# Kernel tuning notes

Measured on AMD Instinct MI355X. Metric: run time of the kernel, lower is better.

## Reference

```python
import jax, jax.numpy as jnp
import numpy as np

EPS = 1e-5
NEG_SLOPE = 0.2
NUM_ITER = 3
C = 32            # channel
LCAPS = 40        # latent_caps_size
LVEC = 40         # latent_vec_size
PCAPS = 1287      # prim_caps_size (937 + 234 + 116)


def conv1d(x, w, stride, pad):
    # x: [B, Cin, L], w: [Cout, Cin, K]
    return jax.lax.conv_general_dilated(
        x, w, window_strides=(stride,), padding=[(pad, pad)],
        dimension_numbers=('NCH', 'OIH', 'NCH'))


def bn_lrelu(x, g, b, m, v):
    # eval-mode BatchNorm1d + LeakyReLU(0.2); x: [B, C, L]
    scale = (g * jax.lax.rsqrt(v + EPS))[None, :, None]
    y = (x - m[None, :, None]) * scale + b[None, :, None]
    return jnp.where(y >= 0, y, NEG_SLOPE * y)


def squash(t):
    sn = jnp.sum(t * t, axis=-1, keepdims=True)
    return sn * t / ((1.0 + sn) * jnp.sqrt(sn))


def setup_inputs() -> dict:
    key = jax.random.key(0)
    ks = jax.random.split(key, 10)
    data = jax.random.normal(ks[0], (32, 1, 4681), jnp.float32)
    conv1_w = 0.1 * jax.random.normal(ks[1], (C, 1, 5), jnp.float32)
    conv2_w = 0.1 * jax.random.normal(ks[2], (C, C, 5), jnp.float32)
    conv3_w = 0.1 * jax.random.normal(ks[3], (C, C, 4), jnp.float32)
    lin_w = 0.1 * jax.random.normal(ks[4], (C, C, 1), jnp.float32)
    bn_gamma = 1.0 + 0.1 * jax.random.normal(ks[5], (4, C), jnp.float32)
    bn_beta = 0.1 * jax.random.normal(ks[6], (4, C), jnp.float32)
    bn_mean = 0.1 * jax.random.normal(ks[7], (4, C), jnp.float32)
    bn_var = 0.5 + jax.random.uniform(ks[8], (4, C), jnp.float32)
    W_caps = 0.01 * jax.random.normal(ks[9], (LCAPS, PCAPS, LVEC, C), jnp.float32)
    return dict(data=data, conv1_w=conv1_w, conv2_w=conv2_w, conv3_w=conv3_w,
                lin_w=lin_w, bn_gamma=bn_gamma, bn_beta=bn_beta,
                bn_mean=bn_mean, bn_var=bn_var, W_caps=W_caps)


def reference(data, conv1_w, conv2_w, conv3_w, lin_w,
              bn_gamma, bn_beta, bn_mean, bn_var, W_caps):
    # OctreeKeyConv (eval mode: BN uses running stats, dropout off)
    x1 = bn_lrelu(conv1d(data, conv1_w, 5, 2), bn_gamma[0], bn_beta[0], bn_mean[0], bn_var[0])  # [B,32,937]
    x2 = bn_lrelu(conv1d(x1, conv2_w, 4, 0), bn_gamma[1], bn_beta[1], bn_mean[1], bn_var[1])    # [B,32,234]
    x3 = bn_lrelu(conv1d(x2, conv3_w, 2, 0), bn_gamma[2], bn_beta[2], bn_mean[2], bn_var[2])    # [B,32,116]
    x = jnp.concatenate([x1, x2, x3], axis=2)                                                    # [B,32,1287]
    x = bn_lrelu(conv1d(x, lin_w, 1, 0), bn_gamma[3], bn_beta[3], bn_mean[3], bn_var[3])
    x = jnp.transpose(x, (0, 2, 1))  # [B, 1287, 32]

    # LatentCapsLayer: u_hat[b,l,p,v] = sum_s W[l,p,v,s] x[b,p,s]
    u_hat = jnp.einsum('lpvs,bps->blpv', W_caps, x)  # [B,40,1287,40]
    u_det = jax.lax.stop_gradient(u_hat)
    B = x.shape[0]
    b_ij = jnp.zeros((B, LCAPS, PCAPS), x.dtype)
    v = None
    for it in range(NUM_ITER):
        c = jax.nn.softmax(b_ij, axis=1)  # softmax over latent caps
        if it == NUM_ITER - 1:
            v = squash(jnp.sum(c[..., None] * u_hat, axis=2, keepdims=True))  # [B,40,1,40]
        else:
            v = squash(jnp.sum(c[..., None] * u_det, axis=2, keepdims=True))
            b_ij = b_ij + jnp.sum(v * u_det, axis=-1)
    latent = jnp.squeeze(v, axis=2)       # [B,40,40]
    return jnp.sum(latent, axis=-1)       # [B,40]
```

## Files before the change

kernel.cpp:

```cpp
#include <hip/hip_runtime.h>

#define EPSB 1e-5f
#define NEG 0.2f

__device__ __forceinline__ float lrelu(float y) { return y >= 0.f ? y : NEG * y; }

typedef const __attribute__((address_space(1))) unsigned int gas1_u32;
typedef __attribute__((address_space(3))) unsigned int as3_u32;
__device__ __forceinline__ void gload16nt(const float* g, float* l) {
  __builtin_amdgcn_global_load_lds((gas1_u32*)g, (as3_u32*)l, 16, 0, 2);
}
#define WAITVM(N) asm volatile("s_waitcnt vmcnt(" #N ")" ::: "memory")

typedef float floatx4 __attribute__((ext_vector_type(4)));
typedef short bf16x8 __attribute__((ext_vector_type(8)));
__device__ __forceinline__ void nt_store4(float4 v, float* addr) {
  floatx4 w = {v.x, v.y, v.z, v.w};
  __builtin_nontemporal_store(w, (floatx4*)addr);
}

__device__ __forceinline__ unsigned short bfr(float f) {
  unsigned int b = __float_as_uint(f);
  return (unsigned short)((b + 0x7FFFu + ((b >> 16) & 1u)) >> 16);
}
__device__ __forceinline__ ushort4 f4bf(floatx4 a) {
  ushort4 r;
  r.x = bfr(a.x); r.y = bfr(a.y); r.z = bfr(a.z); r.w = bfr(a.w);
  return r;
}
__device__ __forceinline__ float4 bf4f(ushort4 h) {
  return make_float4(__uint_as_float((unsigned int)h.x << 16),
                     __uint_as_float((unsigned int)h.y << 16),
                     __uint_as_float((unsigned int)h.z << 16),
                     __uint_as_float((unsigned int)h.w << 16));
}

__device__ __forceinline__ void barrier_nodrain() {
  asm volatile("s_waitcnt lgkmcnt(0)" ::: "memory");
  __builtin_amdgcn_s_barrier();
  __builtin_amdgcn_sched_barrier(0);
}

__global__ __launch_bounds__(256) void k_front(
    const float* __restrict__ data, const float* __restrict__ w1,
    const float* __restrict__ w2, const float* __restrict__ w3,
    const float* __restrict__ lw, const float* __restrict__ bg,
    const float* __restrict__ bb, const float* __restrict__ bm,
    const float* __restrict__ bv, float* __restrict__ xt)
{
  __shared__ float x1s[32][132];
  __shared__ float x2s[32][40];
  __shared__ float x3s[32][20];
  const int b = blockIdx.x >> 3, q = blockIdx.x & 7, t = threadIdx.x;
  const int o1s = (937*q)/8, o1e = (937*(q+1))/8;
  const int o2s = (234*q)/8, o2e = (234*(q+1))/8;
  const int o3s = (116*q)/8, o3e = (116*(q+1))/8;
  int n2s = min(o2s, 2*o3s);
  int n2e = max(o2e, 2*(o3e-1)+4); if (n2e > 234) n2e = 234;
  int n1s = min(o1s, 4*n2s);
  int n1e = max(o1e, 4*(n2e-1)+5); if (n1e > 937) n1e = 937;
  const int w1w = n1e - n1s, w2w = n2e - n2s, w3w = o3e - o3s;

  for (int idx = t; idx < 32*w1w; idx += 256) {
    int c = idx / w1w, j = n1s + idx % w1w;
    float acc = 0.f;
    int base = 5*j - 2;
    #pragma unroll
    for (int k = 0; k < 5; ++k) {
      int pos = base + k;
      float d = (pos >= 0 && pos < 4681) ? data[b*4681 + pos] : 0.f;
      acc += w1[c*5 + k] * d;
    }
    float sc = bg[c] * rsqrtf(bv[c] + EPSB);
    x1s[c][j - n1s] = lrelu((acc - bm[c]) * sc + bb[c]);
  }
  __syncthreads();
  for (int idx = t; idx < 32*w2w; idx += 256) {
    int c = idx / w2w, j = n2s + idx % w2w;
    float acc = 0.f;
    int col = 4*j - n1s;
    for (int ci = 0; ci < 32; ++ci) {
      #pragma unroll
      for (int k = 0; k < 5; ++k) acc += w2[(c*32 + ci)*5 + k] * x1s[ci][col + k];
    }
    float sc = bg[32+c] * rsqrtf(bv[32+c] + EPSB);
    x2s[c][j - n2s] = lrelu((acc - bm[32+c]) * sc + bb[32+c]);
  }
  __syncthreads();
  for (int idx = t; idx < 32*w3w; idx += 256) {
    int c = idx / w3w, j = o3s + idx % w3w;
    float acc = 0.f;
    int col = 2*j - n2s;
    for (int ci = 0; ci < 32; ++ci) {
      #pragma unroll
      for (int k = 0; k < 4; ++k) acc += w3[(c*32 + ci)*4 + k] * x2s[ci][col + k];
    }
    float sc = bg[64+c] * rsqrtf(bv[64+c] + EPSB);
    x3s[c][j - o3s] = lrelu((acc - bm[64+c]) * sc + bb[64+c]);
  }
  __syncthreads();
  const int np1 = o1e - o1s, np2 = o2e - o2s, np3 = o3e - o3s;
  const int np = np1 + np2 + np3;
  for (int idx = t; idx < np*32; idx += 256) {
    int pi = idx >> 5, s = idx & 31;
    float acc = 0.f;
    int p;
    if (pi < np1) {
      int j = o1s + pi; p = j;
      int col = j - n1s;
      for (int ci = 0; ci < 32; ++ci) acc += lw[s*32 + ci] * x1s[ci][col];
    } else if (pi < np1 + np2) {
      int j = o2s + (pi - np1); p = 937 + j;
      int col = j - n2s;
      for (int ci = 0; ci < 32; ++ci) acc += lw[s*32 + ci] * x2s[ci][col];
    } else {
      int j = o3s + (pi - np1 - np2); p = 1171 + j;
      int col = j - o3s;
      for (int ci = 0; ci < 32; ++ci) acc += lw[s*32 + ci] * x3s[ci][col];
    }
    float sc = bg[96+s] * rsqrtf(bv[96+s] + EPSB);
    xt[p*1024 + b*32 + s] = lrelu((acc - bm[96+s]) * sc + bb[96+s]);
  }
}

__global__ __launch_bounds__(256) void k_uhat(
    const float* __restrict__ W, const float* __restrict__ xt,
    unsigned short* __restrict__ ubf, float* __restrict__ s0part)
{
  extern __shared__ float lds[];
  float* wbuf = lds;
  unsigned short* xs_hi = (unsigned short*)(lds + 10240);
  unsigned short* xs_lo = xs_hi + 10240;
  const int t = threadIdx.x;
  const int wv = t >> 6, lane = t & 63;
  const int wi = blockIdx.x*4 + wv;
  const int l = wi % 40, chunk = wi / 40;
  const int p0 = chunk * 8;
  float* myw = wbuf + wv * 2560;
  const float* Wl = W + (size_t)l * 1287 * 1280;
  const int row = lane & 15, g = lane >> 4;

  for (int idx = t; idx < 2048; idx += 256) {
    int pl = idx >> 8, rem = idx & 255;
    int b = rem >> 3, s4 = rem & 7;
    int pg = p0 + pl;
    float4 v = make_float4(0.f, 0.f, 0.f, 0.f);
    if (pg < 1287) v = *(const float4*)(xt + pg*1024 + b*32 + s4*4);
    unsigned int b0 = __float_as_uint(v.x), b1 = __float_as_uint(v.y);
    unsigned int b2 = __float_as_uint(v.z), b3 = __float_as_uint(v.w);
    ushort4 h, lo;
    h.x = (unsigned short)(b0 >> 16); h.y = (unsigned short)(b1 >> 16);
    h.z = (unsigned short)(b2 >> 16); h.w = (unsigned short)(b3 >> 16);
    lo.x = (unsigned short)(__float_as_uint(v.x - __uint_as_float(b0 & 0xffff0000u)) >> 16);
    lo.y = (unsigned short)(__float_as_uint(v.y - __uint_as_float(b1 & 0xffff0000u)) >> 16);
    lo.z = (unsigned short)(__float_as_uint(v.z - __uint_as_float(b2 & 0xffff0000u)) >> 16);
    lo.w = (unsigned short)(__float_as_uint(v.w - __uint_as_float(b3 & 0xffff0000u)) >> 16);
    int off = pl*1280 + b*40 + s4*4;
    *(ushort4*)(xs_hi + off) = h;
    *(ushort4*)(xs_lo + off) = lo;
  }
  #pragma unroll
  for (int i = 0; i < 5; ++i) {
    int gg = i*64 + lane, v = gg >> 3, s4 = (gg & 7) ^ (v & 7);
    gload16nt(Wl + (size_t)p0*1280 + (v*8 + s4)*4, myw + i*256);
  }
  #pragma unroll
  for (int i = 0; i < 5; ++i) {
    int gg = i*64 + lane, v = gg >> 3, s4 = (gg & 7) ^ (v & 7);
    gload16nt(Wl + (size_t)(p0+1)*1280 + (v*8 + s4)*4, myw + 1280 + i*256);
  }
  __syncthreads();

  floatx4 s0acc[2][3];
  #pragma unroll
  for (int mt = 0; mt < 2; ++mt)
    #pragma unroll
    for (int nt = 0; nt < 3; ++nt)
      s0acc[mt][nt] = (floatx4){0.f, 0.f, 0.f, 0.f};

  #pragma unroll
  for (int pp = 0; pp < 8; ++pp) {
    const int p = p0 + pp;
    if (p >= 1287) break;
    if (pp == 1)      WAITVM(11);
    else if (pp >= 2 && pp <= 6) WAITVM(17);
    else if (pp == 7) WAITVM(12);
    const float* wb = myw + (pp & 1)*1280;
    const unsigned short* xh = xs_hi + pp*1280;
    const unsigned short* xl = xs_lo + pp*1280;
    bf16x8 aH[2], aL[2];
    aH[0] = *(const bf16x8*)(xh + row*40 + g*8);
    aH[1] = *(const bf16x8*)(xh + (16 + row)*40 + g*8);
    aL[0] = *(const bf16x8*)(xl + row*40 + g*8);
    aL[1] = *(const bf16x8*)(xl + (16 + row)*40 + g*8);
    floatx4 acc[2][3];
    #pragma unroll
    for (int mt = 0; mt < 2; ++mt)
      #pragma unroll
      for (int nt = 0; nt < 3; ++nt)
        acc[mt][nt] = (floatx4){0.f, 0.f, 0.f, 0.f};
    #pragma unroll
    for (int nt = 0; nt < 3; ++nt) {
      int vq = nt*16 + row;
      bool valid = vq < 40;
      int vv = valid ? vq : 0;
      float4 w0 = *(const float4*)(wb + vv*32 + (((2*g) ^ (vv & 7)) << 2));
      float4 w1 = *(const float4*)(wb + vv*32 + (((2*g + 1) ^ (vv & 7)) << 2));
      float ws[8] = {w0.x, w0.y, w0.z, w0.w, w1.x, w1.y, w1.z, w1.w};
      bf16x8 bH, bL;
      #pragma unroll
      for (int j = 0; j < 8; ++j) {
        unsigned int bits = __float_as_uint(ws[j]);
        unsigned short hs = (unsigned short)(bits >> 16);
        float lf = ws[j] - __uint_as_float(bits & 0xffff0000u);
        unsigned short lsv = (unsigned short)(__float_as_uint(lf) >> 16);
        bH[j] = valid ? (short)hs : (short)0;
        bL[j] = valid ? (short)lsv : (short)0;
      }
      #pragma unroll
      for (int mt = 0; mt < 2; ++mt) {
        acc[mt][nt] = __builtin_amdgcn_mfma_f32_16x16x32_bf16(aH[mt], bH, acc[mt][nt], 0, 0, 0);
        acc[mt][nt] = __builtin_amdgcn_mfma_f32_16x16x32_bf16(aH[mt], bL, acc[mt][nt], 0, 0, 0);
        acc[mt][nt] = __builtin_amdgcn_mfma_f32_16x16x32_bf16(aL[mt], bH, acc[mt][nt], 0, 0, 0);
      }
    }
    if (pp < 6) {
      int psrc = p + 2; if (psrc > 1286) psrc = 1286;
      asm volatile("s_waitcnt lgkmcnt(0)" ::: "memory");
      __builtin_amdgcn_sched_barrier(0);
      #pragma unroll
      for (int i = 0; i < 5; ++i) {
        int gg = i*64 + lane, v = gg >> 3, s4 = (gg & 7) ^ (v & 7);
        gload16nt(Wl + (size_t)psrc*1280 + (v*8 + s4)*4, myw + (pp & 1)*1280 + i*256);
      }
    }
    #pragma unroll
    for (int mt = 0; mt < 2; ++mt)
      #pragma unroll
      for (int nt = 0; nt < 3; ++nt) {
        int vq = nt*16 + row;
        if (vq < 40) {
          int q4 = mt*4 + g;
          *(ushort4*)(ubf + ((size_t)(q4*1287 + p))*6400 + l*160 + vq*4) = f4bf(acc[mt][nt]);
          s0acc[mt][nt] += acc[mt][nt];
        }
      }
  }
  #pragma unroll
  for (int mt = 0; mt < 2; ++mt)
    #pragma unroll
    for (int nt = 0; nt < 3; ++nt) {
      int vq = nt*16 + row;
      if (vq < 40) {
        int q4 = mt*4 + g;
        *(floatx4*)(s0part + (size_t)chunk*51200 + l*1280 + vq*32 + q4*4) = s0acc[mt][nt];
      }
    }
}

__global__ __launch_bounds__(64) void k_squash0(
    const float* __restrict__ s0, float* __restrict__ v0t)
{
  const int b = blockIdx.x / 40, l = blockIdx.x % 40, t = threadIdx.x;
  float s = 0.f;
  if (t < 40) s = s0[(l*40 + t)*32 + b] * (1.f/40.f);
  float sq = s*s;
  #pragma unroll
  for (int d = 1; d < 64; d <<= 1) sq += __shfl_xor(sq, d);
  float scale = sq > 0.f ? sq / ((1.f + sq) * sqrtf(sq)) : 0.f;
  if (t < 40) v0t[((size_t)(b >> 2)*1600 + l*40 + t)*4 + (b & 3)] = s * scale;
}

__global__ __launch_bounds__(64) void k_squash1(
    const float* __restrict__ sred, const float* __restrict__ v0t,
    float* __restrict__ v1t, float* __restrict__ vsum)
{
  const int b = blockIdx.x / 40, l = blockIdx.x % 40, t = threadIdx.x;
  float s = 0.f;
  size_t off = ((size_t)(b >> 2)*1600 + l*40 + t)*4 + (b & 3);
  if (t < 40) s = sred[off];
  float sq = s*s;
  #pragma unroll
  for (int d = 1; d < 64; d <<= 1) sq += __shfl_xor(sq, d);
  float scale = sq > 0.f ? sq / ((1.f + sq) * sqrtf(sq)) : 0.f;
  if (t < 40) {
    float v1 = s * scale;
    v1t[off] = v1;
    vsum[off] = v0t[off] + v1;
  }
}

__global__ __launch_bounds__(64) void k_final(
    const float* __restrict__ sred, float* __restrict__ out)
{
  const int b = blockIdx.x / 40, l = blockIdx.x % 40, t = threadIdx.x;
  float s = 0.f;
  if (t < 40) s = sred[((size_t)(b >> 2)*1600 + l*40 + t)*4 + (b & 3)];
  float sq = s*s, ss = s;
  #pragma unroll
  for (int d = 1; d < 64; d <<= 1) { sq += __shfl_xor(sq, d); ss += __shfl_xor(ss, d); }
  float scale = sq > 0.f ? sq / ((1.f + sq) * sqrtf(sq)) : 0.f;
  if (t == 0) out[b*40 + l] = ss * scale;
}

#define RPC 13
#define NCHUNK 99
__global__ __launch_bounds__(400) void k_route7(
    const unsigned short* __restrict__ ubf, const float* __restrict__ vprev,
    float* __restrict__ spart, int rev)
{
  __shared__ float4 dred[400];
  __shared__ float dot_lds[160];
  __shared__ float c_lds[160];
  const int q4 = blockIdx.x & 7;
  const int chunk0 = blockIdx.x >> 3;
  const int chunk = rev ? (NCHUNK - 1 - chunk0) : chunk0;
  const int t = threadIdx.x;
  const int l = t / 10;
  const int p0 = chunk * RPC;
  const ushort4* u4 = (const ushort4*)ubf;
  const float4* vp4 = (const float4*)vprev + (size_t)q4*1600;

  float4 vv[4], s4[4];
  ushort4 uu[3][4];
  #pragma unroll
  for (int j = 0; j < 4; ++j) {
    vv[j] = vp4[t*4 + j];
    s4[j] = make_float4(0.f, 0.f, 0.f, 0.f);
  }
  {
    const ushort4* up0 = u4 + ((size_t)q4*1287 + p0)*1600;
    const ushort4* up1 = u4 + ((size_t)q4*1287 + p0 + 1)*1600;
    #pragma unroll
    for (int j = 0; j < 4; ++j) { uu[0][j] = up0[t*4 + j]; uu[1][j] = up1[t*4 + j]; }
  }

  #pragma unroll
  for (int pl = 0; pl < RPC; ++pl) {
    const int cur = pl % 3, pf = (pl + 2) % 3;
    const size_t qp = (size_t)q4*1287 + p0 + pl;
    float4 fu[4];
    #pragma unroll
    for (int j = 0; j < 4; ++j) fu[j] = bf4f(uu[cur][j]);
    float4 dp = make_float4(0.f, 0.f, 0.f, 0.f);
    #pragma unroll
    for (int j = 0; j < 4; ++j) {
      dp.x += fu[j].x*vv[j].x; dp.y += fu[j].y*vv[j].y;
      dp.z += fu[j].z*vv[j].z; dp.w += fu[j].w*vv[j].w;
    }
    dred[t] = dp;
    if (pl + 2 < RPC) {
      const ushort4* upn = u4 + (qp + 2)*1600;
      #pragma unroll
      for (int j = 0; j < 4; ++j) uu[pf][j] = upn[t*4 + j];
    }
    barrier_nodrain();
    if (t < 160) {
      const int lr = t >> 2, b4 = t & 3;
      float d = 0.f;
      #pragma unroll
      for (int vq = 0; vq < 10; ++vq)
        d += ((const float*)&dred[lr*10 + vq])[b4];
      dot_lds[b4*40 + lr] = d;
    }
    barrier_nodrain();
    if (t < 256) {
      const int b4 = t >> 6, ll = t & 63;
      float d = (ll < 40) ? dot_lds[b4*40 + ll] : -1e30f;
      float m = d;
      #pragma unroll
      for (int off = 32; off; off >>= 1) m = fmaxf(m, __shfl_xor(m, off));
      float e = expf(d - m);
      float Z = e;
      #pragma unroll
      for (int off = 32; off; off >>= 1) Z += __shfl_xor(Z, off);
      if (ll < 40) c_lds[b4*40 + ll] = e * (1.f / Z);
    }
    barrier_nodrain();
    {
      float c0 = c_lds[l], c1 = c_lds[40 + l], c2 = c_lds[80 + l], c3 = c_lds[120 + l];
      #pragma unroll
      for (int j = 0; j < 4; ++j) {
        s4[j].x += fu[j].x*c0; s4[j].y += fu[j].y*c1;
        s4[j].z += fu[j].z*c2; s4[j].w += fu[j].w*c3;
      }
    }
  }
  float* sp = spart + ((size_t)chunk*8 + q4)*6400;
  #pragma unroll
  for (int j = 0; j < 4; ++j)
    nt_store4(s4[j], sp + (t*4 + j)*4);
}

__global__ __launch_bounds__(256) void k_reduceN(
    const float* __restrict__ src, float* __restrict__ sout, int n)
{
  const int w = blockIdx.x*256 + threadIdx.x;
  float s = 0.f;
  #pragma unroll 4
  for (int c = 0; c < n; ++c)
    s += __builtin_nontemporal_load(src + (size_t)c*51200 + w);
  sout[w] = s;
}

extern "C" void kernel_launch(void* const* d_in, const int* in_sizes, int n_in,
                              void* d_out, int out_size, void* d_ws, size_t ws_size,
                              hipStream_t stream)
{
  const float* data = (const float*)d_in[0];
  const float* w1   = (const float*)d_in[1];
  const float* w2   = (const float*)d_in[2];
  const float* w3   = (const float*)d_in[3];
  const float* lw   = (const float*)d_in[4];
  const float* bg   = (const float*)d_in[5];
  const float* bb   = (const float*)d_in[6];
  const float* bm   = (const float*)d_in[7];
  const float* bv   = (const float*)d_in[8];
  const float* W    = (const float*)d_in[9];
  float* out = (float*)d_out;

  unsigned short* ubf = (unsigned short*)d_ws;
  float* s0     = (float*)d_ws + 32947200;
  float* v0t    = s0 + 51200;
  float* v1t    = v0t + 51200;
  float* s1     = v1t + 51200;
  float* vsum   = s1 + 51200;
  float* xt     = vsum + 51200;
  float* big    = xt + 1317888;
  float* s0part = big;
  float* spart  = big;

  const int KU_LDS = 10240*4 + 2*10240*2;
  hipFuncSetAttribute((const void*)k_uhat,
                      hipFuncAttributeMaxDynamicSharedMemorySize, KU_LDS);

  k_front<<<256, 256, 0, stream>>>(data, w1, w2, w3, lw, bg, bb, bm, bv, xt);
  k_uhat<<<1610, 256, KU_LDS, stream>>>(W, xt, ubf, s0part);
  k_reduceN<<<200, 256, 0, stream>>>(s0part, s0, 161);
  k_squash0<<<1280, 64, 0, stream>>>(s0, v0t);

  k_route7<<<NCHUNK*8, 400, 0, stream>>>(ubf, v0t, spart, 1);
  k_reduceN<<<200, 256, 0, stream>>>(spart, s1, NCHUNK);
  k_squash1<<<1280, 64, 0, stream>>>(s1, v0t, v1t, vsum);

  k_route7<<<NCHUNK*8, 400, 0, stream>>>(ubf, vsum, spart, 0);
  k_reduceN<<<200, 256, 0, stream>>>(spart, s0, NCHUNK);
  k_final<<<1280, 64, 0, stream>>>(s0, out);
}
```

Baseline: 336.1 us.

## Software-pipeline routing loop to cut barriers from three to two per row

Restructures the routing kernel's per-row loop so the dot-product partials for the next row and the weighted accumulation for the previous row overlap with the current row's reduction and softmax. Double-buffered LDS arrays for the partials and the coefficients let each row use two barriers instead of three. This lowers synchronisation stalls across the 400-thread block, at the cost of more registers for the double-buffered converted u values and extra prologue and epilogue code.

```diff
diff --git a/kernel.cpp b/kernel.cpp
--- a/kernel.cpp
+++ b/kernel.cpp
@@ -305,13 +305,13 @@
 
 #define RPC 13
 #define NCHUNK 99
-__global__ __launch_bounds__(400) void k_route7(
+__global__ __launch_bounds__(400) void k_route8(
     const unsigned short* __restrict__ ubf, const float* __restrict__ vprev,
     float* __restrict__ spart, int rev)
 {
-  __shared__ float4 dred[400];
+  __shared__ float4 dred[2][400];
   __shared__ float dot_lds[160];
-  __shared__ float c_lds[160];
+  __shared__ float c_lds[2][160];
   const int q4 = blockIdx.x & 7;
   const int chunk0 = blockIdx.x >> 3;
   const int chunk = rev ? (NCHUNK - 1 - chunk0) : chunk0;
@@ -321,7 +321,7 @@
   const ushort4* u4 = (const ushort4*)ubf;
   const float4* vp4 = (const float4*)vprev + (size_t)q4*1600;
 
-  float4 vv[4], s4[4];
+  float4 vv[4], s4[4], fu[2][4];
   ushort4 uu[3][4];
   #pragma unroll
   for (int j = 0; j < 4; ++j) {
@@ -333,35 +333,42 @@
     const ushort4* up1 = u4 + ((size_t)q4*1287 + p0 + 1)*1600;
     #pragma unroll
     for (int j = 0; j < 4; ++j) { uu[0][j] = up0[t*4 + j]; uu[1][j] = up1[t*4 + j]; }
-  }
+    #pragma unroll
+    for (int j = 0; j < 4; ++j) fu[0][j] = bf4f(uu[0][j]);
+    float4 dp = make_float4(0.f, 0.f, 0.f, 0.f);
+    #pragma unroll
+    for (int j = 0; j < 4; ++j) {
+      dp.x += fu[0][j].x*vv[j].x; dp.y += fu[0][j].y*vv[j].y;
+      dp.z += fu[0][j].z*vv[j].z; dp.w += fu[0][j].w*vv[j].w;
+    }
+    dred[0][t] = dp;
+  }
+  barrier_nodrain();
 
   #pragma unroll
   for (int pl = 0; pl < RPC; ++pl) {
-    const int cur = pl % 3, pf = (pl + 2) % 3;
     const size_t qp = (size_t)q4*1287 + p0 + pl;
-    float4 fu[4];
-    #pragma unroll
-    for (int j = 0; j < 4; ++j) fu[j] = bf4f(uu[cur][j]);
-    float4 dp = make_float4(0.f, 0.f, 0.f, 0.f);
-    #pragma unroll
-    for (int j = 0; j < 4; ++j) {
-      dp.x += fu[j].x*vv[j].x; dp.y += fu[j].y*vv[j].y;
-      dp.z += fu[j].z*vv[j].z; dp.w += fu[j].w*vv[j].w;
-    }
-    dred[t] = dp;
-    if (pl + 2 < RPC) {
-      const ushort4* upn = u4 + (qp + 2)*1600;
-      #pragma unroll
-      for (int j = 0; j < 4; ++j) uu[pf][j] = upn[t*4 + j];
-    }
-    barrier_nodrain();
     if (t < 160) {
       const int lr = t >> 2, b4 = t & 3;
       float d = 0.f;
       #pragma unroll
       for (int vq = 0; vq < 10; ++vq)
-        d += ((const float*)&dred[lr*10 + vq])[b4];
+        d += ((const float*)&dred[pl & 1][lr*10 + vq])[b4];
       dot_lds[b4*40 + lr] = d;
+    }
+    if (pl >= 1) {
+      const float* cl = c_lds[(pl - 1) & 1];
+      float c0 = cl[l], c1 = cl[40 + l], c2 = cl[80 + l], c3 = cl[120 + l];
+      #pragma unroll
+      for (int j = 0; j < 4; ++j) {
+        s4[j].x += fu[(pl - 1) & 1][j].x*c0; s4[j].y += fu[(pl - 1) & 1][j].y*c1;
+        s4[j].z += fu[(pl - 1) & 1][j].z*c2; s4[j].w += fu[(pl - 1) & 1][j].w*c3;
+      }
+    }
+    if (pl + 2 < RPC) {
+      const ushort4* upn = u4 + (qp + 2)*1600;
+      #pragma unroll
+      for (int j = 0; j < 4; ++j) uu[(pl + 2) % 3][j] = upn[t*4 + j];
     }
     barrier_nodrain();
     if (t < 256) {
@@ -374,16 +381,28 @@
       float Z = e;
       #pragma unroll
       for (int off = 32; off; off >>= 1) Z += __shfl_xor(Z, off);
-      if (ll < 40) c_lds[b4*40 + ll] = e * (1.f / Z);
+      if (ll < 40) c_lds[pl & 1][b4*40 + ll] = e * (1.f / Z);
+    }
+    if (pl + 1 < RPC) {
+      #pragma unroll
+      for (int j = 0; j < 4; ++j) fu[(pl + 1) & 1][j] = bf4f(uu[(pl + 1) % 3][j]);
+      float4 dp = make_float4(0.f, 0.f, 0.f, 0.f);
+      #pragma unroll
+      for (int j = 0; j < 4; ++j) {
+        dp.x += fu[(pl + 1) & 1][j].x*vv[j].x; dp.y += fu[(pl + 1) & 1][j].y*vv[j].y;
+        dp.z += fu[(pl + 1) & 1][j].z*vv[j].z; dp.w += fu[(pl + 1) & 1][j].w*vv[j].w;
+      }
+      dred[(pl + 1) & 1][t] = dp;
     }
     barrier_nodrain();
-    {
-      float c0 = c_lds[l], c1 = c_lds[40 + l], c2 = c_lds[80 + l], c3 = c_lds[120 + l];
-      #pragma unroll
-      for (int j = 0; j < 4; ++j) {
-        s4[j].x += fu[j].x*c0; s4[j].y += fu[j].y*c1;
-        s4[j].z += fu[j].z*c2; s4[j].w += fu[j].w*c3;
-      }
+  }
+  {
+    const float* cl = c_lds[(RPC - 1) & 1];
+    float c0 = cl[l], c1 = cl[40 + l], c2 = cl[80 + l], c3 = cl[120 + l];
+    #pragma unroll
+    for (int j = 0; j < 4; ++j) {
+      s4[j].x += fu[(RPC - 1) & 1][j].x*c0; s4[j].y += fu[(RPC - 1) & 1][j].y*c1;
+      s4[j].z += fu[(RPC - 1) & 1][j].z*c2; s4[j].w += fu[(RPC - 1) & 1][j].w*c3;
     }
   }
   float* sp = spart + ((size_t)chunk*8 + q4)*6400;
@@ -439,11 +458,11 @@
   k_reduceN<<<200, 256, 0, stream>>>(s0part, s0, 161);
   k_squash0<<<1280, 64, 0, stream>>>(s0, v0t);
 
-  k_route7<<<NCHUNK*8, 400, 0, stream>>>(ubf, v0t, spart, 1);
+  k_route8<<<NCHUNK*8, 400, 0, stream>>>(ubf, v0t, spart, 1);
   k_reduceN<<<200, 256, 0, stream>>>(spart, s1, NCHUNK);
   k_squash1<<<1280, 64, 0, stream>>>(s1, v0t, v1t, vsum);
 
-  k_route7<<<NCHUNK*8, 400, 0, stream>>>(ubf, vsum, spart, 0);
+  k_route8<<<NCHUNK*8, 400, 0, stream>>>(ubf, vsum, spart, 0);
   k_reduceN<<<200, 256, 0, stream>>>(spart, s0, NCHUNK);
   k_final<<<1280, 64, 0, stream>>>(s0, out);
 }
```

After: 325.9 us. -3.0%, faster.
